# Performance work log

Hardware: AMD Instinct MI355X
Metric: run time of the kernel (lower is better)

The kernel has to match this reference:

```python
import jax, jax.numpy as jnp
import numpy as np

N, C_IN, C_OUT = 8192, 256, 128
TEMP = 1.0
EDGE_P = 0.01  # Bernoulli edge probability -> avg degree ~82


def setup_inputs() -> dict:
    key = jax.random.key(0)
    k_x, k_adj, k_w, k_v0, k_v1 = jax.random.split(key, 5)
    node_feats = jax.random.normal(k_x, (N, C_IN), dtype=jnp.float32)
    adj_matrix = (jax.random.uniform(k_adj, (N, N)) < EDGE_P).astype(jnp.float32)
    lim_w = np.sqrt(6.0 / (C_IN + C_OUT))
    W = jax.random.uniform(k_w, (C_IN, C_OUT), minval=-lim_w, maxval=lim_w, dtype=jnp.float32)
    b = jnp.zeros((C_OUT,), dtype=jnp.float32)
    lim_v = np.sqrt(6.0 / (C_OUT + 1))
    v0 = jax.random.uniform(k_v0, (C_OUT,), minval=-lim_v, maxval=lim_v, dtype=jnp.float32)
    v1 = jax.random.uniform(k_v1, (C_OUT,), minval=-lim_v, maxval=lim_v, dtype=jnp.float32)
    return {"node_feats": node_feats, "adj_matrix": adj_matrix, "W": W, "b": b, "v0": v0, "v1": v1}


def reference(node_feats, adj_matrix, W, b, v0, v1):
    # h: [N, c_out]
    h = node_feats @ W + b
    f1 = h @ v0  # [N]
    f2 = h @ v1  # [N]
    # attn_logits = adj * (f1_i + f2_j); adj==0 entries become exact zeros,
    # which torch's .to_sparse() drops -> sparse softmax normalizes only
    # over edges (adj != 0), and empty rows densify to all-zero rows.
    logits = adj_matrix * (f1[:, None] + f2[None, :])
    vals = (jax.nn.sigmoid(logits) - 0.5) / TEMP
    mask = adj_matrix != 0
    masked = jnp.where(mask, vals, -jnp.inf)
    row_max = jnp.max(masked, axis=1, keepdims=True)
    row_max = jnp.where(jnp.isfinite(row_max), row_max, 0.0)  # guard empty rows
    e = jnp.where(mask, jnp.exp(masked - row_max), 0.0)
    denom = jnp.sum(e, axis=1, keepdims=True)
    attn_probs = e / jnp.maximum(denom, jnp.finfo(e.dtype).tiny)  # empty rows -> 0
    return attn_probs @ h
```

## Files before the change

kernel.cpp:

```cpp
#include <hip/hip_runtime.h>
#include <math.h>

#define NN    8192
#define CIN   256
#define COUT  128
#define MAXEG 256

typedef unsigned uvec4 __attribute__((ext_vector_type(4)));

__global__ __launch_bounds__(256) void k1_gemm(
    const float* __restrict__ X, const float* __restrict__ W,
    const float* __restrict__ b, const float* __restrict__ v0,
    const float* __restrict__ v1,
    float* __restrict__ h, float* __restrict__ f1, float* __restrict__ f2)
{
    __shared__ float Xs[16][32];
    const int tid = threadIdx.x;
    const int ct  = tid & 63;
    const int rg  = tid >> 6;
    const int c   = ct * 2;
    const int row0 = blockIdx.x * 16;

    float acc[4][2] = {{0.f,0.f},{0.f,0.f},{0.f,0.f},{0.f,0.f}};

    for (int kc = 0; kc < CIN; kc += 32) {
        if (tid < 128) {
            const int r = tid >> 3, q = tid & 7;
            const float4 xv = *(const float4*)(X + (size_t)(row0 + r) * CIN + kc + q * 4);
            *(float4*)&Xs[r][q * 4] = xv;
        }
        float2 wv[32];
        #pragma unroll
        for (int kk = 0; kk < 32; ++kk)
            wv[kk] = *(const float2*)(W + (size_t)(kc + kk) * COUT + c);
        __syncthreads();

        #pragma unroll
        for (int rr = 0; rr < 4; ++rr) {
            const int lr = rg * 4 + rr;
            #pragma unroll
            for (int k4 = 0; k4 < 8; ++k4) {
                const float4 xv = *(const float4*)&Xs[lr][k4 * 4];
                acc[rr][0] += xv.x * wv[k4*4+0].x; acc[rr][1] += xv.x * wv[k4*4+0].y;
                acc[rr][0] += xv.y * wv[k4*4+1].x; acc[rr][1] += xv.y * wv[k4*4+1].y;
                acc[rr][0] += xv.z * wv[k4*4+2].x; acc[rr][1] += xv.z * wv[k4*4+2].y;
                acc[rr][0] += xv.w * wv[k4*4+3].x; acc[rr][1] += xv.w * wv[k4*4+3].y;
            }
        }
        __syncthreads();
    }

    const float b0 = b[c], b1 = b[c+1];
    const float v00 = v0[c], v01 = v0[c+1];
    const float v10 = v1[c], v11 = v1[c+1];

    #pragma unroll
    for (int rr = 0; rr < 4; ++rr) {
        const int row = row0 + rg * 4 + rr;
        const float h0 = acc[rr][0] + b0;
        const float h1 = acc[rr][1] + b1;
        *(float2*)(h + (size_t)row * COUT + c) = make_float2(h0, h1);
        float p0 = h0 * v00 + h1 * v01;
        float p1 = h0 * v10 + h1 * v11;
        #pragma unroll
        for (int off = 32; off; off >>= 1) {
            p0 += __shfl_down(p0, off, 64);
            p1 += __shfl_down(p1, off, 64);
        }
        if (ct == 0) { f1[row] = p0; f2[row] = p1; }
    }
}

__global__ __launch_bounds__(256) void k2_fused(
    const float* __restrict__ adj, const float* __restrict__ h,
    const float* __restrict__ f1, const float* __restrict__ f2,
    float* __restrict__ out)
{
    __shared__ unsigned short sjl[4][MAXEG];
    __shared__ float vl[4][MAXEG];

    const int tid  = threadIdx.x;
    const int wid  = tid >> 6;
    const int lane = tid & 63;
    const int row  = blockIdx.x * 4 + wid;
    const uvec4* rowp = (const uvec4*)(adj + (size_t)row * NN) + lane;

    unsigned wcnt = 0;
    uvec4 va[8], vb[8];

    auto process = [&](const uvec4 (&v)[8], const int b) {
        unsigned lm = 0;
        #pragma unroll
        for (int it = 0; it < 8; ++it) {
            const unsigned m4 = ((v[it].x >> 23) & 1u) | ((v[it].y >> 22) & 2u) |
                                ((v[it].z >> 21) & 4u) | ((v[it].w >> 20) & 8u);
            lm |= m4 << (it * 4);
        }
        const int lc = __popc(lm);
        int pre = lc;
        #pragma unroll
        for (int off = 1; off < 64; off <<= 1) {
            const int t = __shfl_up(pre, off, 64);
            if (lane >= off) pre += t;
        }
        unsigned basep = wcnt + (unsigned)(pre - lc);
        wcnt += (unsigned)__shfl(pre, 63, 64);
        unsigned mm = lm;
        while (mm) {
            const int bit = __builtin_ctz(mm);
            mm &= mm - 1;
            const unsigned j = (unsigned)((b * 512 + (bit >> 2) * 64 + lane) * 4 + (bit & 3));
            if (basep < MAXEG) sjl[wid][basep] = (unsigned short)j;
            ++basep;
        }
    };

    #pragma unroll
    for (int it = 0; it < 8; ++it) va[it] = rowp[0 * 512 + it * 64];
    #pragma unroll
    for (int it = 0; it < 8; ++it) vb[it] = rowp[1 * 512 + it * 64];
    process(va, 0);
    #pragma unroll
    for (int it = 0; it < 8; ++it) va[it] = rowp[2 * 512 + it * 64];
    process(vb, 1);
    #pragma unroll
    for (int it = 0; it < 8; ++it) vb[it] = rowp[3 * 512 + it * 64];
    process(va, 2);
    process(vb, 3);

    const int n = min((int)wcnt, MAXEG);
    const int c = lane * 2;
    if (n == 0) {
        *(float2*)(out + (size_t)row * COUT + c) = make_float2(0.f, 0.f);
        return;
    }

    asm volatile("s_waitcnt lgkmcnt(0)" ::: "memory");

    const float f1i = f1[row];
    float m = -1e30f;
    #pragma unroll
    for (int q = 0; q < 4; ++q) {
        const int p = lane + q * 64;
        if (p < n) {
            const float x = f1i + f2[sjl[wid][p]];
            const float s = 1.f / (1.f + __expf(-x)) - 0.5f;
            vl[wid][p] = s;
            m = fmaxf(m, s);
        }
    }
    #pragma unroll
    for (int off = 32; off; off >>= 1) m = fmaxf(m, __shfl_xor(m, off, 64));

    float ssum = 0.f;
    #pragma unroll
    for (int q = 0; q < 4; ++q) {
        const int p = lane + q * 64;
        if (p < n) {
            const float e = __expf(vl[wid][p] - m);
            vl[wid][p] = e;
            ssum += e;
        }
    }
    #pragma unroll
    for (int off = 32; off; off >>= 1) ssum += __shfl_xor(ssum, off, 64);
    const float inv = 1.f / ssum;
    asm volatile("s_waitcnt lgkmcnt(0)" ::: "memory");

    float ax = 0.f, ay = 0.f;
    int p = 0;
    for (; p + 7 < n; p += 8) {
        int   jj[8];
        float ww[8];
        float2 aa[8];
        #pragma unroll
        for (int u = 0; u < 8; ++u) { jj[u] = sjl[wid][p + u]; ww[u] = vl[wid][p + u]; }
        #pragma unroll
        for (int u = 0; u < 8; ++u) aa[u] = *(const float2*)(h + (size_t)jj[u] * COUT + c);
        #pragma unroll
        for (int u = 0; u < 8; ++u) { ax += ww[u] * aa[u].x; ay += ww[u] * aa[u].y; }
    }
    for (; p < n; ++p) {
        const int   j = sjl[wid][p];
        const float w = vl[wid][p];
        const float2 a = *(const float2*)(h + (size_t)j * COUT + c);
        ax += w * a.x;
        ay += w * a.y;
    }
    *(float2*)(out + (size_t)row * COUT + c) = make_float2(ax * inv, ay * inv);
}

extern "C" void kernel_launch(void* const* d_in, const int* in_sizes, int n_in,
                              void* d_out, int out_size, void* d_ws, size_t ws_size,
                              hipStream_t stream) {
    const float* X   = (const float*)d_in[0];
    const float* adj = (const float*)d_in[1];
    const float* W   = (const float*)d_in[2];
    const float* b   = (const float*)d_in[3];
    const float* v0  = (const float*)d_in[4];
    const float* v1  = (const float*)d_in[5];
    float* out = (float*)d_out;

    float* h  = (float*)d_ws;
    float* f1 = h + (size_t)NN * COUT;
    float* f2 = f1 + NN;

    k1_gemm<<<NN / 16, 256, 0, stream>>>(X, W, b, v0, v1, h, f1, f2);
    k2_fused<<<NN / 4, 256, 0, stream>>>(adj, h, f1, f2, out);
}
```

Baseline: 94.33 us.

## Split adjacency scan into standalone bitmap kernel before attention aggregation

Adds a separate streaming kernel that compresses the dense float adjacency matrix into a bit-per-edge bitmap with fully coalesced wide loads over a grid-stride layout. The attention kernel then reads only 1 KB of bitmap per row and builds its neighbour list with popcount and prefix scan, replacing the per-row 32 KB float scan fused with the gather. The aim is to separate the bandwidth-bound adjacency read from the latency-bound gather so each can run at full occupancy. The cost is an extra kernel launch plus a workspace write and read of the bitmap.

```diff
diff --git a/kernel.cpp b/kernel.cpp
--- a/kernel.cpp
+++ b/kernel.cpp
@@ -5,6 +5,7 @@
 #define CIN   256
 #define COUT  128
 #define MAXEG 256
+#define P1BLK 2048
 
 typedef unsigned uvec4 __attribute__((ext_vector_type(4)));
 
@@ -71,8 +72,24 @@
     }
 }
 
-__global__ __launch_bounds__(256) void k2_fused(
-    const float* __restrict__ adj, const float* __restrict__ h,
+__global__ __launch_bounds__(256) void k_bitmap(
+    const uvec4* __restrict__ adj4, unsigned char* __restrict__ bm)
+{
+    const unsigned gtid = blockIdx.x * 256 + threadIdx.x;
+    #pragma unroll 4
+    for (int it = 0; it < 16; ++it) {
+        const size_t base = (size_t)it * (P1BLK * 256) + gtid;
+        const uvec4 a = adj4[base * 2];
+        const uvec4 b = adj4[base * 2 + 1];
+        const unsigned m =
+            (a.x ? 1u   : 0u) | (a.y ? 2u   : 0u) | (a.z ? 4u   : 0u) | (a.w ? 8u   : 0u) |
+            (b.x ? 16u  : 0u) | (b.y ? 32u  : 0u) | (b.z ? 64u  : 0u) | (b.w ? 128u : 0u);
+        bm[base] = (unsigned char)m;
+    }
+}
+
+__global__ __launch_bounds__(256) void k2_attn(
+    const unsigned* __restrict__ bm, const float* __restrict__ h,
     const float* __restrict__ f1, const float* __restrict__ f2,
     float* __restrict__ out)
 {
@@ -83,69 +100,49 @@
     const int wid  = tid >> 6;
     const int lane = tid & 63;
     const int row  = blockIdx.x * 4 + wid;
-    const uvec4* rowp = (const uvec4*)(adj + (size_t)row * NN) + lane;
-
-    unsigned wcnt = 0;
-    uvec4 va[8], vb[8];
-
-    auto process = [&](const uvec4 (&v)[8], const int b) {
-        unsigned lm = 0;
-        #pragma unroll
-        for (int it = 0; it < 8; ++it) {
-            const unsigned m4 = ((v[it].x >> 23) & 1u) | ((v[it].y >> 22) & 2u) |
-                                ((v[it].z >> 21) & 4u) | ((v[it].w >> 20) & 8u);
-            lm |= m4 << (it * 4);
-        }
-        const int lc = __popc(lm);
-        int pre = lc;
-        #pragma unroll
-        for (int off = 1; off < 64; off <<= 1) {
-            const int t = __shfl_up(pre, off, 64);
-            if (lane >= off) pre += t;
-        }
-        unsigned basep = wcnt + (unsigned)(pre - lc);
-        wcnt += (unsigned)__shfl(pre, 63, 64);
-        unsigned mm = lm;
+    const int c    = lane * 2;
+
+    const uvec4 w4 = ((const uvec4*)(bm + (size_t)row * 256))[lane];
+    unsigned wa[4] = { w4.x, w4.y, w4.z, w4.w };
+
+    const int lc = __popc(wa[0]) + __popc(wa[1]) + __popc(wa[2]) + __popc(wa[3]);
+    int pre = lc;
+    #pragma unroll
+    for (int off = 1; off < 64; off <<= 1) {
+        const int t = __shfl_up(pre, off, 64);
+        if (lane >= off) pre += t;
+    }
+    unsigned p = (unsigned)(pre - lc);
+    const int n0 = __shfl(pre, 63, 64);
+    const int n  = min(n0, MAXEG);
+
+    const int jb = lane * 128;
+    #pragma unroll
+    for (int k = 0; k < 4; ++k) {
+        unsigned mm = wa[k];
         while (mm) {
             const int bit = __builtin_ctz(mm);
             mm &= mm - 1;
-            const unsigned j = (unsigned)((b * 512 + (bit >> 2) * 64 + lane) * 4 + (bit & 3));
-            if (basep < MAXEG) sjl[wid][basep] = (unsigned short)j;
-            ++basep;
-        }
-    };
-
-    #pragma unroll
-    for (int it = 0; it < 8; ++it) va[it] = rowp[0 * 512 + it * 64];
-    #pragma unroll
-    for (int it = 0; it < 8; ++it) vb[it] = rowp[1 * 512 + it * 64];
-    process(va, 0);
-    #pragma unroll
-    for (int it = 0; it < 8; ++it) va[it] = rowp[2 * 512 + it * 64];
-    process(vb, 1);
-    #pragma unroll
-    for (int it = 0; it < 8; ++it) vb[it] = rowp[3 * 512 + it * 64];
-    process(va, 2);
-    process(vb, 3);
-
-    const int n = min((int)wcnt, MAXEG);
-    const int c = lane * 2;
+            if (p < MAXEG) sjl[wid][p] = (unsigned short)(jb + k * 32 + bit);
+            ++p;
+        }
+    }
+
     if (n == 0) {
         *(float2*)(out + (size_t)row * COUT + c) = make_float2(0.f, 0.f);
         return;
     }
-
     asm volatile("s_waitcnt lgkmcnt(0)" ::: "memory");
 
     const float f1i = f1[row];
     float m = -1e30f;
     #pragma unroll
     for (int q = 0; q < 4; ++q) {
-        const int p = lane + q * 64;
-        if (p < n) {
-            const float x = f1i + f2[sjl[wid][p]];
+        const int pp = lane + q * 64;
+        if (pp < n) {
+            const float x = f1i + f2[sjl[wid][pp]];
             const float s = 1.f / (1.f + __expf(-x)) - 0.5f;
-            vl[wid][p] = s;
+            vl[wid][pp] = s;
             m = fmaxf(m, s);
         }
     }
@@ -155,10 +152,10 @@
     float ssum = 0.f;
     #pragma unroll
     for (int q = 0; q < 4; ++q) {
-        const int p = lane + q * 64;
-        if (p < n) {
-            const float e = __expf(vl[wid][p] - m);
-            vl[wid][p] = e;
+        const int pp = lane + q * 64;
+        if (pp < n) {
+            const float e = __expf(vl[wid][pp] - m);
+            vl[wid][pp] = e;
             ssum += e;
         }
     }
@@ -168,21 +165,21 @@
     asm volatile("s_waitcnt lgkmcnt(0)" ::: "memory");
 
     float ax = 0.f, ay = 0.f;
-    int p = 0;
-    for (; p + 7 < n; p += 8) {
+    int q = 0;
+    for (; q + 7 < n; q += 8) {
         int   jj[8];
         float ww[8];
         float2 aa[8];
         #pragma unroll
-        for (int u = 0; u < 8; ++u) { jj[u] = sjl[wid][p + u]; ww[u] = vl[wid][p + u]; }
+        for (int u = 0; u < 8; ++u) { jj[u] = sjl[wid][q + u]; ww[u] = vl[wid][q + u]; }
         #pragma unroll
         for (int u = 0; u < 8; ++u) aa[u] = *(const float2*)(h + (size_t)jj[u] * COUT + c);
         #pragma unroll
         for (int u = 0; u < 8; ++u) { ax += ww[u] * aa[u].x; ay += ww[u] * aa[u].y; }
     }
-    for (; p < n; ++p) {
-        const int   j = sjl[wid][p];
-        const float w = vl[wid][p];
+    for (; q < n; ++q) {
+        const int   j = sjl[wid][q];
+        const float w = vl[wid][q];
         const float2 a = *(const float2*)(h + (size_t)j * COUT + c);
         ax += w * a.x;
         ay += w * a.y;
@@ -201,10 +198,12 @@
     const float* v1  = (const float*)d_in[5];
     float* out = (float*)d_out;
 
-    float* h  = (float*)d_ws;
-    float* f1 = h + (size_t)NN * COUT;
-    float* f2 = f1 + NN;
+    float*         h  = (float*)d_ws;
+    float*         f1 = h + (size_t)NN * COUT;
+    float*         f2 = f1 + NN;
+    unsigned char* bm = (unsigned char*)(f2 + NN);
 
     k1_gemm<<<NN / 16, 256, 0, stream>>>(X, W, b, v0, v1, h, f1, f2);
-    k2_fused<<<NN / 4, 256, 0, stream>>>(adj, h, f1, f2, out);
-}
+    k_bitmap<<<P1BLK, 256, 0, stream>>>((const uvec4*)adj, bm);
+    k2_attn<<<NN / 4, 256, 0, stream>>>((const unsigned*)bm, h, f1, f2, out);
+}
```

Measured after the change: 98.00 us. +3.9%, slower.
